# Optimization experiments

Hardware: AMD Instinct MI355X
Metric: run time of the kernel (lower is better)

## Reference

```python
import jax, jax.numpy as jnp
import numpy as np

GRID = 8
NMS_SIZE = 4
TOP_K = 1000
DET_THRESH = 0.015
EPS = 1e-5


def _conv(x, w, b):
    # NCHW, OIHW, SAME padding, stride 1
    y = jax.lax.conv_general_dilated(x, w, (1, 1), 'SAME',
                                     dimension_numbers=('NCHW', 'OIHW', 'NCHW'))
    return y + b[None, :, None, None]


def _bn(x, gamma, beta, mean, var):
    inv = gamma / jnp.sqrt(var + EPS)
    return x * inv[None, :, None, None] + (beta - mean * inv)[None, :, None, None]


def _pixel_shuffle1(x, r):
    # x: [B, r*r, h, w] -> [B, h*r, w*r]  (C_out = 1, squeezed)
    B, C, h, w = x.shape
    x = x.reshape(B, r, r, h, w)
    x = x.transpose(0, 3, 1, 4, 2)  # B, h, r, w, r
    return x.reshape(B, h * r, w * r)


def _box_nms_batched(prob):
    # local-max suppression in a (2*size+1) window + keep top_k scores
    win = 2 * NMS_SIZE + 1
    pooled = jax.lax.reduce_window(prob, -jnp.inf, jax.lax.max,
                                   (1, win, win), (1, 1, 1), 'SAME')
    keep = jnp.where(prob == pooled, prob, 0.0)
    B = keep.shape[0]
    flat = keep.reshape(B, -1)
    kth = jax.lax.top_k(flat, TOP_K)[0][:, -1]  # [B]
    flat = jnp.where(flat >= kth[:, None], flat, 0.0)
    return flat.reshape(prob.shape)


def setup_inputs() -> dict:
    key = jax.random.key(0)
    ks = jax.random.split(key, 5)
    c_in, c_hid = 128, 256
    c_out = GRID * GRID + 1  # 65
    x = jax.random.normal(ks[0], (32, c_in, 60, 80), dtype=jnp.float32)
    wa = jax.random.normal(ks[1], (c_hid, c_in, 3, 3), dtype=jnp.float32) * 0.05
    ba = jnp.zeros((c_hid,), jnp.float32)
    ga = jnp.ones((c_hid,), jnp.float32)
    bta = jnp.zeros((c_hid,), jnp.float32)
    ma = jnp.zeros((c_hid,), jnp.float32)
    va = jnp.ones((c_hid,), jnp.float32)
    wb = jax.random.normal(ks[2], (c_out, c_hid, 1, 1), dtype=jnp.float32) * 0.05
    bb = jnp.zeros((c_out,), jnp.float32)
    gb = jnp.ones((c_out,), jnp.float32)
    btb = jnp.zeros((c_out,), jnp.float32)
    mb = jnp.zeros((c_out,), jnp.float32)
    vb = jnp.ones((c_out,), jnp.float32)
    return {"x": x, "wa": wa, "ba": ba, "ga": ga, "bta": bta, "ma": ma, "va": va,
            "wb": wb, "bb": bb, "gb": gb, "btb": btb, "mb": mb, "vb": vb}


def reference(x, wa, ba, ga, bta, ma, va, wb, bb, gb, btb, mb, vb):
    # convPa: conv3x3 + BN + ReLU
    h = jax.nn.relu(_bn(_conv(x, wa, ba), ga, bta, ma, va))
    # convPb: conv1x1 + BN (no activation)
    logits = _bn(_conv(h, wb, bb), gb, btb, mb, vb)  # [B, 65, h, w]
    # NOTE: original code computes softmax then overwrites it with raw logits
    # (x_prob = self.softmax(x); x_prob = x[:, :-1]) -- we reproduce that bug.
    _ = jax.nn.softmax(logits, axis=1)
    prob = _pixel_shuffle1(logits[:, :-1, :, :], GRID)  # [B, H, W]
    prob_nms = _box_nms_batched(prob)
    pred = (prob_nms >= DET_THRESH).astype(jnp.int32)
    return logits, prob, prob_nms, pred
```

## Files before the change

kernel.cpp:

```cpp
#include <hip/hip_runtime.h>
#include <math.h>

typedef short s16x8 __attribute__((ext_vector_type(8)));
typedef float f32x4 __attribute__((ext_vector_type(4)));
typedef unsigned short u16;

#define B_    32
#define CIN   128
#define CHID  256
#define H_    60
#define W_    80
#define COUT  65
#define HP    480
#define WP    640
#define TOPK  1000
#define CAND_MAX 8192
#define DET_THRESH 0.015f

#define LOGITS_N (B_*COUT*H_*W_)
#define PROB_N   (B_*HP*WP)
#define PROB_OFF (LOGITS_N)
#define NMS_OFF  (PROB_OFF + PROB_N)
#define PRED_OFF (NMS_OFF + PROB_N)

#define WB_FN    442368
#define SA_OFF   WB_FN
#define TA_OFF   (SA_OFF + 256)
#define TB_OFF   (TA_OFF + 256)
#define WB1_FN   30720
#define WB1_OFF  (TB_OFF + 128)
#define H_OFF    (WB1_OFF + WB1_FN)
#define H_N      (B_*H_*W_*CHID)
#define CAND_OFF (H_OFF + H_N)
#define CNT_OFF  (CAND_OFF + B_*CAND_MAX)
#define CNT_N    (32*32)
#define KTH_OFF  (CNT_OFF + CNT_N)
#define WT_N     (CHID*CIN*9)
#define WB1_U16N 61440

#define AROW  58
#define APLN  6264

__device__ __forceinline__ u16 f2bf(float x) {
    unsigned u = __float_as_uint(x);
    return (u16)((u + 0x7fffu + ((u >> 16) & 1u)) >> 16);
}
__device__ __forceinline__ float bf2f(u16 h) {
    return __uint_as_float(((unsigned)h) << 16);
}

#define MFMA16 __builtin_amdgcn_mfma_f32_16x16x32_bf16

__global__ void prep_kernel(const float* __restrict__ wa,
                            const float* __restrict__ ba, const float* __restrict__ ga,
                            const float* __restrict__ bta, const float* __restrict__ ma,
                            const float* __restrict__ va,
                            const float* __restrict__ wb, const float* __restrict__ bb,
                            const float* __restrict__ gb, const float* __restrict__ btb,
                            const float* __restrict__ mb, const float* __restrict__ vb,
                            u16* __restrict__ WBo,
                            float* __restrict__ sa, float* __restrict__ ta,
                            float* __restrict__ tb, u16* __restrict__ WB1o)
{
    int gid = blockIdx.x * 256 + threadIdx.x;
    if (gid < WT_N) {
        int icl = gid & 31;
        int ocl = (gid >> 5) & 63;
        int rest = gid >> 11;
        int tap = rest % 9;
        int cq = rest / 9;
        int icc = cq & 3, ocq = cq >> 2;
        float v = wa[(((ocq * 64 + ocl) * CIN) + icc * 32 + icl) * 9 + tap];
        u16 hh = f2bf(v); float r1 = v - bf2f(hh);
        u16 mm2 = f2bf(r1); float r2 = r1 - bf2f(mm2);
        u16 ll = f2bf(r2);
        size_t base = ((size_t)(((ocq * 4 + icc) * 9 + tap) * 3)) * 2048
                      + ocl * 32 + icl;
        WBo[base] = hh;
        WBo[base + 2048] = mm2;
        WBo[base + 4096] = ll;
    } else if (gid < WT_N + 256) {
        int oc = gid - WT_N;
        float inv = ga[oc] / sqrtf(va[oc] + 1e-5f);
        sa[oc] = inv;
        ta[oc] = (ba[oc] - ma[oc]) * inv + bta[oc];
    } else if (gid < WT_N + 256 + COUT) {
        int oc = gid - (WT_N + 256);
        float inv = gb[oc] / sqrtf(vb[oc] + 1e-5f);
        tb[oc] = (bb[oc] - mb[oc]) * inv + btb[oc];
    } else if (gid < WT_N + 256 + COUT + WB1_U16N) {
        int idx = gid - (WT_N + 256 + COUT);
        int within = idx & 511;
        int j = within & 7;
        int lane = within >> 3;
        int chunk = idx >> 9;
        int plane = chunk % 3;
        int kc = (chunk / 3) & 7;
        int ocf = chunk / 24;
        int oc = ocf * 16 + (lane & 15);
        int k = kc * 32 + (lane >> 4) * 8 + j;
        float v = 0.f;
        if (oc < COUT) {
            float inv = gb[oc] / sqrtf(vb[oc] + 1e-5f);
            v = wb[oc * CHID + k] * inv;
        }
        u16 hh = f2bf(v); float r1 = v - bf2f(hh);
        u16 mm2 = f2bf(r1); float r2 = r1 - bf2f(mm2);
        u16 ll = f2bf(r2);
        WB1o[idx] = (plane == 0) ? hh : (plane == 1) ? mm2 : ll;
    }
}

__global__ __launch_bounds__(256, 2) void conv3_kernel(const float* __restrict__ x,
                                                       const u16* __restrict__ WB,
                                                       const float* __restrict__ sa,
                                                       const float* __restrict__ ta,
                                                       float* __restrict__ h)
{
    __shared__ __align__(16) u16 xsA[3 * APLN];

    int d = blockIdx.x;
    int o = (d & 7) * 300 + (d >> 3);
    int tile = o % 75;
    int b = o / 75;
    int ty = tile / 5, tx = tile % 5;
    int y0 = ty * 4, x0 = tx * 16;

    int t = threadIdx.x;
    int wv = __builtin_amdgcn_readfirstlane(t >> 6);
    int lane = t & 63;
    int cx = lane & 15;
    int kg = lane >> 4;
    int icl0 = kg * 8;

    const float* xb = x + (size_t)b * CIN * H_ * W_;

    int goff[14];
#pragma unroll
    for (int j = 0; j < 14; ++j) {
        int e = t + j * 256;
        int go = -1;
        if (e < 3456) {
            int xx = e % 18;
            int yy = (e / 18) % 6;
            int icl = e / 108;
            int gy = y0 + yy - 1, gx = x0 + xx - 1;
            if (gy >= 0 && gy < H_ && gx >= 0 && gx < W_)
                go = icl * (H_ * W_) + gy * W_ + gx;
        }
        goff[j] = go;
    }

    f32x4 acc[4][4];
#pragma unroll
    for (int pb = 0; pb < 4; ++pb)
#pragma unroll
        for (int f = 0; f < 4; ++f) acc[pb][f] = (f32x4)(0.f);

    float xr[14];
#pragma unroll
    for (int j = 0; j < 14; ++j)
        xr[j] = (goff[j] >= 0) ? xb[goff[j]] : 0.f;

#pragma unroll 1
    for (int icc = 0; icc < 4; ++icc) {
        __syncthreads();
#pragma unroll
        for (int j = 0; j < 14; ++j) {
            int e = t + j * 256;
            if (e < 3456) {
                int xx = e % 18;
                int yy = (e / 18) % 6;
                int icl = e / 108;
                float v = xr[j];
                u16 hh = f2bf(v); float r1 = v - bf2f(hh);
                u16 mm2 = f2bf(r1); float r2 = r1 - bf2f(mm2);
                u16 ll = f2bf(r2);
                int pos = yy * 18 + xx;
                int wu = pos * AROW + ((icl >> 3) << 4) + (icl & 7);
                xsA[wu] = hh;
                xsA[APLN + wu] = mm2;
                xsA[2 * APLN + wu] = ll;
            }
        }
        __syncthreads();

        if (icc < 3) {
            const float* xc = xb + (icc + 1) * 32 * (H_ * W_);
#pragma unroll
            for (int j = 0; j < 14; ++j)
                if (goff[j] >= 0) xr[j] = xc[goff[j]];
        }

#pragma unroll 1
        for (int tap = 0; tap < 9; ++tap) {
            int dy = tap / 3, dx = tap - dy * 3;

            const u16* bb_ = WB + ((size_t)(((wv * 4 + icc) * 9 + tap) * 3)) * 2048;
            s16x8 Bh[4], Bm[4], Bl[4];
#pragma unroll
            for (int f = 0; f < 4; ++f) {
                int bu = (f * 16 + cx) * 32 + icl0;
                Bh[f] = *(const s16x8*)&bb_[bu];
                Bm[f] = *(const s16x8*)&bb_[2048 + bu];
                Bl[f] = *(const s16x8*)&bb_[4096 + bu];
            }

#pragma unroll
            for (int pb = 0; pb < 4; ++pb) {
                int pos = (pb + dy) * 18 + cx + dx;
                int au = pos * AROW + (kg << 4);
                s16x8 Ah = *(const s16x8*)&xsA[au];
                s16x8 Am = *(const s16x8*)&xsA[APLN + au];
                s16x8 Al = *(const s16x8*)&xsA[2 * APLN + au];
#pragma unroll
                for (int f = 0; f < 4; ++f) {
                    acc[pb][f] = MFMA16(Ah, Bh[f], acc[pb][f], 0, 0, 0);
                    acc[pb][f] = MFMA16(Ah, Bm[f], acc[pb][f], 0, 0, 0);
                    acc[pb][f] = MFMA16(Am, Bh[f], acc[pb][f], 0, 0, 0);
                    acc[pb][f] = MFMA16(Ah, Bl[f], acc[pb][f], 0, 0, 0);
                    acc[pb][f] = MFMA16(Am, Bm[f], acc[pb][f], 0, 0, 0);
                    acc[pb][f] = MFMA16(Al, Bh[f], acc[pb][f], 0, 0, 0);
                }
            }
        }
    }

#pragma unroll
    for (int f = 0; f < 4; ++f) {
        int oc = wv * 64 + f * 16 + cx;
        float s_ = sa[oc], t_ = ta[oc];
#pragma unroll
        for (int pb = 0; pb < 4; ++pb) {
            int y = y0 + pb;
#pragma unroll
            for (int r = 0; r < 4; ++r) {
                int xc2 = x0 + kg * 4 + r;
                size_t addr = ((size_t)(b * (H_ * W_) + y * W_ + xc2)) * CHID + oc;
                h[addr] = fmaxf(fmaf(acc[pb][f][r], s_, t_), 0.f);
            }
        }
    }
}

__global__ __launch_bounds__(256) void conv1_kernel(const float* __restrict__ h,
                                                    const u16* __restrict__ WB1,
                                                    const float* __restrict__ tb,
                                                    float* __restrict__ logits,
                                                    float* __restrict__ prob)
{
    int t = threadIdx.x;
    int wv = t >> 6;
    int lane = t & 63;
    int px0 = blockIdx.x * 128 + wv * 32;
    int k0l = (lane >> 4) * 8;

    const float* hp0 = h + (size_t)(px0 + (lane & 15)) * CHID + k0l;
    const float* hp1 = hp0 + 16 * CHID;

    f32x4 acc0[5], acc1[5];
#pragma unroll
    for (int f = 0; f < 5; ++f) { acc0[f] = (f32x4)(0.f); acc1[f] = (f32x4)(0.f); }

#pragma unroll 1
    for (int kc = 0; kc < 8; ++kc) {
        s16x8 Ah0, Am0, Al0, Ah1, Am1, Al1;
        {
            float4 a0 = *(const float4*)(hp0 + kc * 32);
            float4 a1 = *(const float4*)(hp0 + kc * 32 + 4);
            float av[8] = {a0.x, a0.y, a0.z, a0.w, a1.x, a1.y, a1.z, a1.w};
#pragma unroll
            for (int j = 0; j < 8; ++j) {
                u16 hh = f2bf(av[j]); float r1 = av[j] - bf2f(hh);
                u16 mm2 = f2bf(r1); float r2 = r1 - bf2f(mm2);
                Ah0[j] = (short)hh; Am0[j] = (short)mm2; Al0[j] = (short)f2bf(r2);
            }
        }
        {
            float4 a0 = *(const float4*)(hp1 + kc * 32);
            float4 a1 = *(const float4*)(hp1 + kc * 32 + 4);
            float av[8] = {a0.x, a0.y, a0.z, a0.w, a1.x, a1.y, a1.z, a1.w};
#pragma unroll
            for (int j = 0; j < 8; ++j) {
                u16 hh = f2bf(av[j]); float r1 = av[j] - bf2f(hh);
                u16 mm2 = f2bf(r1); float r2 = r1 - bf2f(mm2);
                Ah1[j] = (short)hh; Am1[j] = (short)mm2; Al1[j] = (short)f2bf(r2);
            }
        }
#pragma unroll
        for (int f = 0; f < 5; ++f) {
            const u16* bbase = WB1 + ((size_t)(f * 8 + kc) * 3) * 512 + lane * 8;
            s16x8 Bh = *(const s16x8*)bbase;
            s16x8 Bm = *(const s16x8*)(bbase + 512);
            s16x8 Bl = *(const s16x8*)(bbase + 1024);
            acc0[f] = MFMA16(Ah0, Bh, acc0[f], 0, 0, 0);
            acc0[f] = MFMA16(Ah0, Bm, acc0[f], 0, 0, 0);
            acc0[f] = MFMA16(Am0, Bh, acc0[f], 0, 0, 0);
            acc0[f] = MFMA16(Ah0, Bl, acc0[f], 0, 0, 0);
            acc0[f] = MFMA16(Am0, Bm, acc0[f], 0, 0, 0);
            acc0[f] = MFMA16(Al0, Bh, acc0[f], 0, 0, 0);
            acc1[f] = MFMA16(Ah1, Bh, acc1[f], 0, 0, 0);
            acc1[f] = MFMA16(Ah1, Bm, acc1[f], 0, 0, 0);
            acc1[f] = MFMA16(Am1, Bh, acc1[f], 0, 0, 0);
            acc1[f] = MFMA16(Ah1, Bl, acc1[f], 0, 0, 0);
            acc1[f] = MFMA16(Am1, Bm, acc1[f], 0, 0, 0);
            acc1[f] = MFMA16(Al1, Bh, acc1[f], 0, 0, 0);
        }
    }

#define C1_EPI(ACC, PXB)                                                        \
    {                                                                           \
        int pxm = (PXB) + (lane >> 4) * 4;                                      \
        _Pragma("unroll")                                                       \
        for (int f = 0; f < 5; ++f) {                                           \
            int oc = f * 16 + (lane & 15);                                      \
            if (oc < COUT) {                                                    \
                float tbv = tb[oc];                                             \
                _Pragma("unroll")                                               \
                for (int r = 0; r < 4; ++r) {                                   \
                    int p = pxm + r;                                            \
                    int b = p / (H_ * W_);                                      \
                    int yx = p % (H_ * W_);                                     \
                    float val = ACC[f][r] + tbv;                                \
                    logits[((size_t)(b * COUT + oc)) * (H_ * W_) + yx] = val;   \
                    if (oc < 64) {                                              \
                        int y = yx / W_, xx = yx % W_;                          \
                        prob[(size_t)b * (HP * WP) + (y * 8 + (oc >> 3)) * WP   \
                             + xx * 8 + (oc & 7)] = val;                        \
                    }                                                           \
                }                                                               \
            }                                                                   \
        }                                                                       \
    }

    C1_EPI(acc0, px0)
    C1_EPI(acc1, px0 + 16)
#undef C1_EPI
}

__global__ __launch_bounds__(256) void nms_kernel(const float* __restrict__ prob,
                                                  float* __restrict__ keep_out,
                                                  float* __restrict__ cand,
                                                  int* __restrict__ cnt)
{
    __shared__ float xs[40][40];
    __shared__ float rmax[40][32];
    __shared__ float clist[1024];
    __shared__ int csh;
    __shared__ int gbase;

    int bid = blockIdx.x;
    int tx = bid % 20;
    int ty = (bid / 20) % 15;
    int b = bid / 300;
    const float* pb = prob + (size_t)b * (HP * WP);
    int t = threadIdx.x;

    if (t == 0) csh = 0;

    for (int idx = t; idx < 1600; idx += 256) {
        int c = idx % 40, r = idx / 40;
        int gy = ty * 32 - 4 + r;
        int gx = tx * 32 - 4 + c;
        float v = -INFINITY;
        if (gy >= 0 && gy < HP && gx >= 0 && gx < WP) v = pb[gy * WP + gx];
        xs[r][c] = v;
    }
    __syncthreads();

    for (int idx = t; idx < 1280; idx += 256) {
        int c = idx & 31, r = idx >> 5;
        float m = xs[r][c];
#pragma unroll
        for (int d = 1; d < 9; ++d) m = fmaxf(m, xs[r][c + d]);
        rmax[r][c] = m;
    }
    __syncthreads();

    for (int idx = t; idx < 1024; idx += 256) {
        int c = idx & 31, ro = idx >> 5;
        float m = rmax[ro][c];
#pragma unroll
        for (int d = 1; d < 9; ++d) m = fmaxf(m, rmax[ro + d][c]);
        float v = xs[ro + 4][c + 4];
        float keep = (v == m) ? v : 0.f;
        keep_out[(size_t)b * (HP * WP) + (ty * 32 + ro) * WP + tx * 32 + c] = keep;
        if (keep > 0.f) {
            int i = atomicAdd(&csh, 1);
            clist[i] = keep;
        }
    }
    __syncthreads();

    int m = csh;
    if (m > 0) {
        if (t == 0) gbase = atomicAdd(&cnt[b * 32], m);
        __syncthreads();
        int gb = gbase;
        for (int i = t; i < m; i += 256) {
            int dst = gb + i;
            if (dst < CAND_MAX) cand[b * CAND_MAX + dst] = clist[i];
        }
    }
}

__global__ __launch_bounds__(256) void select_kernel(const float* __restrict__ cand,
                                                     const int* __restrict__ cnt,
                                                     float* __restrict__ kth)
{
    __shared__ unsigned hist[256];
    __shared__ unsigned sh_prefix, sh_K;

    int b = blockIdx.x;
    int t = threadIdx.x;
    int n = cnt[b * 32];
    if (n > CAND_MAX) n = CAND_MAX;
    if (n < TOPK) {
        if (t == 0) kth[b] = 0.f;
        return;
    }
    if (t == 0) { sh_prefix = 0u; sh_K = TOPK; }
    __syncthreads();
    const float* cb = cand + b * CAND_MAX;

    for (int pass = 3; pass >= 0; --pass) {
        hist[t] = 0u;
        __syncthreads();
        unsigned prefix = sh_prefix;
        unsigned himask = (pass == 3) ? 0u : (0xFFFFFFFFu << ((pass + 1) * 8));
        for (int i = t; i < n; i += 256) {
            unsigned u = __float_as_uint(cb[i]);
            if ((u & himask) == prefix)
                atomicAdd(&hist[(u >> (pass * 8)) & 255], 1u);
        }
        __syncthreads();
        if (t == 0) {
            unsigned K = sh_K, cum = 0;
            int sel = 0;
            for (int v2 = 255; v2 >= 0; --v2) {
                if (cum + hist[v2] >= K) { sel = v2; sh_K = K - cum; break; }
                cum += hist[v2];
            }
            sh_prefix = prefix | ((unsigned)sel << (pass * 8));
        }
        __syncthreads();
    }
    if (t == 0) kth[b] = __uint_as_float(sh_prefix);
}

__global__ __launch_bounds__(256) void thresh_kernel(const float* __restrict__ keep,
                                                     const float* __restrict__ kth,
                                                     float* __restrict__ prob_nms,
                                                     float* __restrict__ pred)
{
    int i4 = blockIdx.x * 256 + threadIdx.x;
    int b = i4 / (HP * WP / 4);
    float tv = kth[b];
    float4 v = ((const float4*)keep)[i4];
    float4 o;
    o.x = (v.x >= tv) ? v.x : 0.f;
    o.y = (v.y >= tv) ? v.y : 0.f;
    o.z = (v.z >= tv) ? v.z : 0.f;
    o.w = (v.w >= tv) ? v.w : 0.f;
    ((float4*)prob_nms)[i4] = o;
    float4 pr;
    pr.x = (o.x >= DET_THRESH) ? 1.f : 0.f;
    pr.y = (o.y >= DET_THRESH) ? 1.f : 0.f;
    pr.z = (o.z >= DET_THRESH) ? 1.f : 0.f;
    pr.w = (o.w >= DET_THRESH) ? 1.f : 0.f;
    ((float4*)pred)[i4] = pr;
}

extern "C" void kernel_launch(void* const* d_in, const int* in_sizes, int n_in,
                              void* d_out, int out_size, void* d_ws, size_t ws_size,
                              hipStream_t stream) {
    const float* x   = (const float*)d_in[0];
    const float* wa  = (const float*)d_in[1];
    const float* ba  = (const float*)d_in[2];
    const float* ga  = (const float*)d_in[3];
    const float* bta = (const float*)d_in[4];
    const float* ma  = (const float*)d_in[5];
    const float* va  = (const float*)d_in[6];
    const float* wb  = (const float*)d_in[7];
    const float* bb  = (const float*)d_in[8];
    const float* gb  = (const float*)d_in[9];
    const float* btb = (const float*)d_in[10];
    const float* mb  = (const float*)d_in[11];
    const float* vb  = (const float*)d_in[12];

    float* out = (float*)d_out;
    float* ws  = (float*)d_ws;

    u16*   WB   = (u16*)ws;
    float* sa   = ws + SA_OFF;
    float* ta   = ws + TA_OFF;
    float* tbv  = ws + TB_OFF;
    u16*   WB1  = (u16*)(ws + WB1_OFF);
    float* h    = ws + H_OFF;
    float* cand = ws + CAND_OFF;
    int*   cnt  = (int*)(ws + CNT_OFF);
    float* kth  = ws + KTH_OFF;

    hipMemsetAsync((void*)cnt, 0, CNT_N * sizeof(int), stream);

    {
        int total = WT_N + 256 + COUT + WB1_U16N;
        prep_kernel<<<(total + 255) / 256, 256, 0, stream>>>(
            wa, ba, ga, bta, ma, va, wb, bb, gb, btb, mb, vb, WB, sa, ta, tbv, WB1);
    }

    conv3_kernel<<<2400, 256, 0, stream>>>(x, WB, sa, ta, h);

    conv1_kernel<<<(B_ * H_ * W_) / 128, 256, 0, stream>>>(
        h, WB1, tbv, out, out + PROB_OFF);

    nms_kernel<<<32 * 15 * 20, 256, 0, stream>>>(
        out + PROB_OFF, out + NMS_OFF, cand, cnt);

    select_kernel<<<B_, 256, 0, stream>>>(cand, cnt, kth);

    thresh_kernel<<<(PROB_N / 4) / 256, 256, 0, stream>>>(
        out + NMS_OFF, kth, out + NMS_OFF, out + PRED_OFF);
}
```

Before: 592.1 us.

## Fuse 1x1 conv into 3x3 conv kernel via shared-memory hidden tile

The 1x1 convolution (conv1_kernel) is folded into the end of the 3x3 conv kernel. The BN+ReLU hidden activations for each 64-pixel tile go into shared memory (reusing the input staging buffer) instead of a global 256-channel intermediate. Each wave then runs the split-bf16 MFMA 1x1 conv over its 16 pixels and writes logits and pixel-shuffled prob directly. This removes the large global write and read of h and one launch, at the cost of more shared memory, two extra barriers, and a longer tail per conv3 block.

```diff
diff --git a/kernel.cpp b/kernel.cpp
--- a/kernel.cpp
+++ b/kernel.cpp
@@ -29,9 +29,7 @@
 #define TB_OFF   (TA_OFF + 256)
 #define WB1_FN   30720
 #define WB1_OFF  (TB_OFF + 128)
-#define H_OFF    (WB1_OFF + WB1_FN)
-#define H_N      (B_*H_*W_*CHID)
-#define CAND_OFF (H_OFF + H_N)
+#define CAND_OFF (WB1_OFF + WB1_FN)
 #define CNT_OFF  (CAND_OFF + B_*CAND_MAX)
 #define CNT_N    (32*32)
 #define KTH_OFF  (CNT_OFF + CNT_N)
@@ -40,6 +38,7 @@
 
 #define AROW  58
 #define APLN  6264
+#define HROW  260
 
 __device__ __forceinline__ u16 f2bf(float x) {
     unsigned u = __float_as_uint(x);
@@ -113,11 +112,16 @@
 
 __global__ __launch_bounds__(256, 2) void conv3_kernel(const float* __restrict__ x,
                                                        const u16* __restrict__ WB,
+                                                       const u16* __restrict__ WB1,
                                                        const float* __restrict__ sa,
                                                        const float* __restrict__ ta,
-                                                       float* __restrict__ h)
+                                                       const float* __restrict__ tb,
+                                                       float* __restrict__ logits,
+                                                       float* __restrict__ prob)
 {
-    __shared__ __align__(16) u16 xsA[3 * APLN];
+    __shared__ __align__(16) u16 shm[2 * HROW * 64];
+    u16* xsA = shm;
+    float* hs = (float*)shm;
 
     int d = blockIdx.x;
     int o = (d & 7) * 300 + (d >> 3);
@@ -226,65 +230,41 @@
         }
     }
 
+    __syncthreads();
+
 #pragma unroll
     for (int f = 0; f < 4; ++f) {
         int oc = wv * 64 + f * 16 + cx;
         float s_ = sa[oc], t_ = ta[oc];
 #pragma unroll
         for (int pb = 0; pb < 4; ++pb) {
-            int y = y0 + pb;
 #pragma unroll
             for (int r = 0; r < 4; ++r) {
-                int xc2 = x0 + kg * 4 + r;
-                size_t addr = ((size_t)(b * (H_ * W_) + y * W_ + xc2)) * CHID + oc;
-                h[addr] = fmaxf(fmaf(acc[pb][f][r], s_, t_), 0.f);
-            }
-        }
-    }
-}
-
-__global__ __launch_bounds__(256) void conv1_kernel(const float* __restrict__ h,
-                                                    const u16* __restrict__ WB1,
-                                                    const float* __restrict__ tb,
-                                                    float* __restrict__ logits,
-                                                    float* __restrict__ prob)
-{
-    int t = threadIdx.x;
-    int wv = t >> 6;
-    int lane = t & 63;
-    int px0 = blockIdx.x * 128 + wv * 32;
-    int k0l = (lane >> 4) * 8;
-
-    const float* hp0 = h + (size_t)(px0 + (lane & 15)) * CHID + k0l;
-    const float* hp1 = hp0 + 16 * CHID;
-
-    f32x4 acc0[5], acc1[5];
-#pragma unroll
-    for (int f = 0; f < 5; ++f) { acc0[f] = (f32x4)(0.f); acc1[f] = (f32x4)(0.f); }
+                int lpx = pb * 16 + kg * 4 + r;
+                hs[lpx * HROW + oc] = fmaxf(fmaf(acc[pb][f][r], s_, t_), 0.f);
+            }
+        }
+    }
+    __syncthreads();
+
+    const float* hrow = hs + (size_t)(wv * 16 + cx) * HROW + kg * 8;
+
+    f32x4 acc1[5];
+#pragma unroll
+    for (int f = 0; f < 5; ++f) acc1[f] = (f32x4)(0.f);
 
 #pragma unroll 1
     for (int kc = 0; kc < 8; ++kc) {
-        s16x8 Ah0, Am0, Al0, Ah1, Am1, Al1;
+        s16x8 Ah, Am, Al;
         {
-            float4 a0 = *(const float4*)(hp0 + kc * 32);
-            float4 a1 = *(const float4*)(hp0 + kc * 32 + 4);
+            float4 a0 = *(const float4*)(hrow + kc * 32);
+            float4 a1 = *(const float4*)(hrow + kc * 32 + 4);
             float av[8] = {a0.x, a0.y, a0.z, a0.w, a1.x, a1.y, a1.z, a1.w};
 #pragma unroll
             for (int j = 0; j < 8; ++j) {
                 u16 hh = f2bf(av[j]); float r1 = av[j] - bf2f(hh);
                 u16 mm2 = f2bf(r1); float r2 = r1 - bf2f(mm2);
-                Ah0[j] = (short)hh; Am0[j] = (short)mm2; Al0[j] = (short)f2bf(r2);
-            }
-        }
-        {
-            float4 a0 = *(const float4*)(hp1 + kc * 32);
-            float4 a1 = *(const float4*)(hp1 + kc * 32 + 4);
-            float av[8] = {a0.x, a0.y, a0.z, a0.w, a1.x, a1.y, a1.z, a1.w};
-#pragma unroll
-            for (int j = 0; j < 8; ++j) {
-                u16 hh = f2bf(av[j]); float r1 = av[j] - bf2f(hh);
-                u16 mm2 = f2bf(r1); float r2 = r1 - bf2f(mm2);
-                Ah1[j] = (short)hh; Am1[j] = (short)mm2; Al1[j] = (short)f2bf(r2);
+                Ah[j] = (short)hh; Am[j] = (short)mm2; Al[j] = (short)f2bf(r2);
             }
         }
 #pragma unroll
@@ -293,49 +273,37 @@
             s16x8 Bh = *(const s16x8*)bbase;
             s16x8 Bm = *(const s16x8*)(bbase + 512);
             s16x8 Bl = *(const s16x8*)(bbase + 1024);
-            acc0[f] = MFMA16(Ah0, Bh, acc0[f], 0, 0, 0);
-            acc0[f] = MFMA16(Ah0, Bm, acc0[f], 0, 0, 0);
-            acc0[f] = MFMA16(Am0, Bh, acc0[f], 0, 0, 0);
-            acc0[f] = MFMA16(Ah0, Bl, acc0[f], 0, 0, 0);
-            acc0[f] = MFMA16(Am0, Bm, acc0[f], 0, 0, 0);
-            acc0[f] = MFMA16(Al0, Bh, acc0[f], 0, 0, 0);
-            acc1[f] = MFMA16(Ah1, Bh, acc1[f], 0, 0, 0);
-            acc1[f] = MFMA16(Ah1, Bm, acc1[f], 0, 0, 0);
-            acc1[f] = MFMA16(Am1, Bh, acc1[f], 0, 0, 0);
-            acc1[f] = MFMA16(Ah1, Bl, acc1[f], 0, 0, 0);
-            acc1[f] = MFMA16(Am1, Bm, acc1[f], 0, 0, 0);
-            acc1[f] = MFMA16(Al1, Bh, acc1[f], 0, 0, 0);
-        }
-    }
-
-#define C1_EPI(ACC, PXB)                                                        \
-    {                                                                           \
-        int pxm = (PXB) + (lane >> 4) * 4;                                      \
-        _Pragma("unroll")                                                       \
-        for (int f = 0; f < 5; ++f) {                                           \
-            int oc = f * 16 + (lane & 15);                                      \
-            if (oc < COUT) {                                                    \
-                float tbv = tb[oc];                                             \
-                _Pragma("unroll")                                               \
-                for (int r = 0; r < 4; ++r) {                                   \
-                    int p = pxm + r;                                            \
-                    int b = p / (H_ * W_);                                      \
-                    int yx = p % (H_ * W_);                                     \
-                    float val = ACC[f][r] + tbv;                                \
-                    logits[((size_t)(b * COUT + oc)) * (H_ * W_) + yx] = val;   \
-                    if (oc < 64) {                                              \
-                        int y = yx / W_, xx = yx % W_;                          \
-                        prob[(size_t)b * (HP * WP) + (y * 8 + (oc >> 3)) * WP   \
-                             + xx * 8 + (oc & 7)] = val;                        \
-                    }                                                           \
-                }                                                               \
-            }                                                                   \
-        }                                                                       \
-    }
-
-    C1_EPI(acc0, px0)
-    C1_EPI(acc1, px0 + 16)
-#undef C1_EPI
+            acc1[f] = MFMA16(Ah, Bh, acc1[f], 0, 0, 0);
+            acc1[f] = MFMA16(Ah, Bm, acc1[f], 0, 0, 0);
+            acc1[f] = MFMA16(Am, Bh, acc1[f], 0, 0, 0);
+            acc1[f] = MFMA16(Ah, Bl, acc1[f], 0, 0, 0);
+            acc1[f] = MFMA16(Am, Bm, acc1[f], 0, 0, 0);
+            acc1[f] = MFMA16(Al, Bh, acc1[f], 0, 0, 0);
+        }
+    }
+
+    {
+        int y = y0 + wv;
+        int rowbase = b * (H_ * W_) + y * W_;
+#pragma unroll
+        for (int f = 0; f < 5; ++f) {
+            int oc = f * 16 + cx;
+            if (oc < COUT) {
+                float tbv = tb[oc];
+#pragma unroll
+                for (int r = 0; r < 4; ++r) {
+                    int xx = x0 + kg * 4 + r;
+                    float val = acc1[f][r] + tbv;
+                    logits[((size_t)(b * COUT + oc)) * (H_ * W_) + y * W_ + xx] = val;
+                    if (oc < 64) {
+                        prob[(size_t)b * (HP * WP) + (y * 8 + (oc >> 3)) * WP
+                             + xx * 8 + (oc & 7)] = val;
+                    }
+                }
+            }
+        }
+        (void)rowbase;
+    }
 }
 
 __global__ __launch_bounds__(256) void nms_kernel(const float* __restrict__ prob,
@@ -496,7 +464,6 @@
     float* ta   = ws + TA_OFF;
     float* tbv  = ws + TB_OFF;
     u16*   WB1  = (u16*)(ws + WB1_OFF);
-    float* h    = ws + H_OFF;
     float* cand = ws + CAND_OFF;
     int*   cnt  = (int*)(ws + CNT_OFF);
     float* kth  = ws + KTH_OFF;
@@ -509,10 +476,8 @@
             wa, ba, ga, bta, ma, va, wb, bb, gb, btb, mb, vb, WB, sa, ta, tbv, WB1);
     }
 
-    conv3_kernel<<<2400, 256, 0, stream>>>(x, WB, sa, ta, h);
-
-    conv1_kernel<<<(B_ * H_ * W_) / 128, 256, 0, stream>>>(
-        h, WB1, tbv, out, out + PROB_OFF);
+    conv3_kernel<<<2400, 256, 0, stream>>>(
+        x, WB, WB1, sa, ta, tbv, out, out + PROB_OFF);
 
     nms_kernel<<<32 * 15 * 20, 256, 0, stream>>>(
         out + PROB_OFF, out + NMS_OFF, cand, cnt);
```

Result: slower. 628.1 us (+6.1%).
